# Performance work log

Measured on AMD Instinct MI355X. Metric: run time of the kernel, lower is better.

The kernel has to match this reference:

```python
import jax, jax.numpy as jnp
import numpy as np
import math

SEQLEN, DIM, N_HEADS = 2048, 4096, 32
HEAD_DIM = DIM // N_HEADS
NEG_INF = -1e30  # exp underflows to exactly 0, same effect as -inf without NaN risk


def setup_inputs() -> dict:
    key = jax.random.key(0)
    ks = jax.random.split(key, 7)
    scale = 1.0 / math.sqrt(DIM)
    x = jax.random.normal(ks[0], (SEQLEN, DIM), dtype=jnp.float32)
    weight_q = jax.random.normal(ks[1], (DIM, DIM), dtype=jnp.float32) * scale
    weight_k = jax.random.normal(ks[2], (DIM, DIM), dtype=jnp.float32) * scale
    weight_v = jax.random.normal(ks[3], (DIM, DIM), dtype=jnp.float32) * scale
    weight_o = jax.random.normal(ks[4], (DIM, DIM), dtype=jnp.float32) * scale
    # RoPE frequencies: freqs_cis = exp(i * t * theta_j), standard LLaMA schedule
    inv_freq = 1.0 / (10000.0 ** (np.arange(0, HEAD_DIM, 2, dtype=np.float32) / HEAD_DIM))
    angles = np.arange(SEQLEN, dtype=np.float32)[:, None] * inv_freq[None, :]  # [S, hd/2]
    freqs_cos = jnp.asarray(np.cos(angles), dtype=jnp.float32)
    freqs_sin = jnp.asarray(np.sin(angles), dtype=jnp.float32)
    # additive causal mask [S, S]
    mask = jnp.where(jnp.triu(jnp.ones((SEQLEN, SEQLEN), dtype=bool), k=1), NEG_INF, 0.0).astype(jnp.float32)
    return {"x": x, "weight_q": weight_q, "weight_k": weight_k, "weight_v": weight_v,
            "weight_o": weight_o, "freqs_cos": freqs_cos, "freqs_sin": freqs_sin,
            "mask": mask, "start_pos": 0}


def _apply_rope(t, cos, sin):
    # t: [S, H, hd]; cos/sin: [S, hd/2]
    tr = t.reshape(*t.shape[:-1], -1, 2)           # [S, H, hd/2, 2]
    t_re, t_im = tr[..., 0], tr[..., 1]
    c = cos[:, None, :]
    s = sin[:, None, :]
    out_re = t_re * c - t_im * s
    out_im = t_re * s + t_im * c
    return jnp.stack([out_re, out_im], axis=-1).reshape(t.shape)


def reference(x, weight_q, weight_k, weight_v, weight_o, freqs_cos, freqs_sin, mask, start_pos):
    S, D = x.shape
    hd = freqs_cos.shape[-1] * 2
    H = D // hd
    # the per-head double loop over wq[j][i] is exactly a full [D,D] projection
    xq = (x @ weight_q).reshape(S, H, hd)
    xk = (x @ weight_k).reshape(S, H, hd)
    xv = (x @ weight_v).reshape(S, H, hd)
    xq = _apply_rope(xq, freqs_cos, freqs_sin)
    xk = _apply_rope(xk, freqs_cos, freqs_sin)
    # start_pos == 0 prefill: cache slice == freshly computed keys/values
    scores = jnp.einsum('shd,thd->hst', xq, xk) / jnp.sqrt(jnp.float32(hd))
    scores = scores + mask[None, :, :]
    probs = jax.nn.softmax(scores.astype(jnp.float32), axis=-1).astype(xq.dtype)
    qkv = jnp.einsum('hst,thd->shd', probs, xv).reshape(S, D)
    return qkv @ weight_o
```

## Files before the change

### kernel.cpp

```cpp
#include <hip/hip_runtime.h>
#include <hip/hip_bf16.h>
#include <type_traits>

typedef __hip_bfloat16 bf16;
typedef __attribute__((ext_vector_type(8))) short s8v;
typedef __attribute__((ext_vector_type(4))) short s4v;
typedef __attribute__((ext_vector_type(4))) float f4v;

#define MFMA16(A, B, C) __builtin_amdgcn_mfma_f32_16x16x32_bf16((A), (B), (C), 0, 0, 0)

constexpr int SEQ = 2048;
constexpr int DIM = 4096;
constexpr int NH  = 32;
constexpr int HD  = 128;

__device__ __forceinline__ short f2bs(float f) {
    __hip_bfloat16_raw r = __float2bfloat16(f);
    return (short)r.x;
}

__device__ __forceinline__ void ld_g2l(const bf16* g, bf16* l) {
    __builtin_amdgcn_global_load_lds(
        (const __attribute__((address_space(1))) void*)g,
        (__attribute__((address_space(3))) void*)l, 16, 0, 0);
}

__global__ void convert_bf16(const float* __restrict__ s, bf16* __restrict__ d) {
    int i = blockIdx.x * blockDim.x + threadIdx.x;
    float4 f = ((const float4*)s)[i];
    s4v o;
    o[0] = f2bs(f.x); o[1] = f2bs(f.y); o[2] = f2bs(f.z); o[3] = f2bs(f.w);
    *(s4v*)(d + (size_t)i * 4) = o;
}

__global__ __launch_bounds__(256) void convt_bf16(const float* __restrict__ src,
                                                  bf16* __restrict__ dst,
                                                  int R, int C) {
    __shared__ float t[64][65];
    const int c0 = blockIdx.x * 64, r0 = blockIdx.y * 64;
    const int tid = threadIdx.x;
    const int lr = tid >> 4;
    const int lc = (tid & 15) * 4;
#pragma unroll
    for (int i = 0; i < 4; i++) {
        float4 f = *(const float4*)(src + (size_t)(r0 + lr + 16 * i) * C + c0 + lc);
        t[lr + 16 * i][lc]     = f.x;
        t[lr + 16 * i][lc + 1] = f.y;
        t[lr + 16 * i][lc + 2] = f.z;
        t[lr + 16 * i][lc + 3] = f.w;
    }
    __syncthreads();
    const int oc = tid >> 2;
#pragma unroll
    for (int i = 0; i < 2; i++) {
        int rr = (tid & 3) * 8 + 32 * i;
        s8v o;
#pragma unroll
        for (int e = 0; e < 8; e++) o[e] = f2bs(t[rr + e][oc]);
        *(s8v*)(dst + (size_t)(c0 + oc) * R + r0 + rr) = o;
    }
}

template <typename CT>
__global__ __launch_bounds__(512, 2) void gemm_256(const bf16* __restrict__ A,
                                                   const bf16* __restrict__ Bt,
                                                   CT* __restrict__ C,
                                                   int K, size_t cstride) {
    __shared__ bf16 As_[2][256 * 64];
    __shared__ bf16 Bs_[2][256 * 64];
    const int tid  = threadIdx.x;
    const int lane = tid & 63;
    const int wv   = tid >> 6;
    const int m16  = lane & 15;
    const int quad = lane >> 4;
    const int wm   = wv >> 2, wn = wv & 3;

    const int NBN = (int)gridDim.x;
    const int lin = (int)(blockIdx.y * gridDim.x + blockIdx.x);
    const int nw8 = (int)(gridDim.x * gridDim.y) >> 3;
    const int nv  = (lin & 7) * nw8 + (lin >> 3);
    const int bm  = nv / NBN;
    const int bn  = nv - bm * NBN;

    const bf16* Ab = A  + (size_t)bm * 256 * K;
    const bf16* Bb = Bt + (size_t)bn * 256 * K;

    const int row0 = tid >> 3;
    const int gc8  = ((tid & 7) ^ (row0 & 7)) * 8;
    const int dst0 = wv * 512;
    const int dst1 = 4096 + wv * 512;

    const int aB  = (wm * 128 + m16) * 64;
    const int bB  = (wn * 64 + m16) * 64;
    const int swz = m16 & 7;
    const int c0k = ((0 + quad) ^ swz) * 8;
    const int c1k = ((4 + quad) ^ swz) * 8;

    const int NT = K >> 6;

    f4v acc[8][4] = {};
    s8v aR[4][2], bR[4][2];

#define STAGEH(gb, lb) do { \
        ld_g2l((gb) + (size_t)row0 * K + gc8, (lb) + dst0); \
        ld_g2l((gb) + (size_t)(row0 + 64) * K + gc8, (lb) + dst1); } while (0)
#define LDA_(i, ks)  aR[i][ks] = *(const s8v*)(Ac + aB + (i) * 1024 + ((ks) ? c1k : c0k))
#define LDAU_(i, ks) aR[i][ks] = *(const s8v*)(Ac + aB + (i) * 1024 + 4096 + ((ks) ? c1k : c0k))
#define LDB_(j, ks)  bR[j][ks] = *(const s8v*)(Bc + bB + (j) * 1024 + ((ks) ? c1k : c0k))
#define MMQ(ai, i, j) do { acc[ai][j] = MFMA16(aR[i][0], bR[j][0], acc[ai][j]); \
                           acc[ai][j] = MFMA16(aR[i][1], bR[j][1], acc[ai][j]); } while (0)
#define BARX()  __builtin_amdgcn_s_barrier()
#define LGKM0() do { asm volatile("s_waitcnt lgkmcnt(0)" ::: "memory"); \
                     __builtin_amdgcn_sched_barrier(0); } while (0)

    STAGEH(Ab, As_[0]); STAGEH(Ab + (size_t)128 * K, As_[0] + 8192);
    STAGEH(Bb, Bs_[0]); STAGEH(Bb + (size_t)128 * K, Bs_[0] + 8192);
    STAGEH(Ab + 64, As_[1]); STAGEH(Ab + (size_t)128 * K + 64, As_[1] + 8192);
    STAGEH(Bb + 64, Bs_[1]); STAGEH(Bb + (size_t)128 * K + 64, Bs_[1] + 8192);
    asm volatile("s_waitcnt vmcnt(8)" ::: "memory");
    __builtin_amdgcn_sched_barrier(0);
    BARX();

    for (int t = 0; t < NT; ++t) {
        const int cur = t & 1;
        const bf16* Ac = As_[cur];
        const bf16* Bc = Bs_[cur];
        const bool more = (t + 2 < NT);
        const int k2 = (t + 2) << 6;

        LDA_(0, 0); LDA_(0, 1); LDA_(1, 0); LDA_(1, 1);
        LDA_(2, 0); LDA_(2, 1); LDA_(3, 0); LDA_(3, 1);
        LDB_(0, 0); LDB_(0, 1); LDB_(1, 0); LDB_(1, 1);
        BARX(); LGKM0();
        __builtin_amdgcn_s_setprio(1);
        MMQ(0, 0, 0); MMQ(0, 0, 1); MMQ(1, 1, 0); MMQ(1, 1, 1);
        MMQ(2, 2, 0); MMQ(2, 2, 1); MMQ(3, 3, 0); MMQ(3, 3, 1);
        __builtin_amdgcn_s_setprio(0);
        BARX();

        LDB_(2, 0); LDB_(2, 1); LDB_(3, 0); LDB_(3, 1);
        BARX(); LGKM0();
        __builtin_amdgcn_s_setprio(1);
        MMQ(0, 0, 2); MMQ(0, 0, 3); MMQ(1, 1, 2); MMQ(1, 1, 3);
        MMQ(2, 2, 2); MMQ(2, 2, 3); MMQ(3, 3, 2); MMQ(3, 3, 3);
        __builtin_amdgcn_s_setprio(0);
        BARX();

        LDAU_(0, 0); LDAU_(0, 1); LDAU_(1, 0); LDAU_(1, 1);
        LDAU_(2, 0); LDAU_(2, 1); LDAU_(3, 0); LDAU_(3, 1);
        if (more) {
            STAGEH(Bb + k2, Bs_[cur]);
            STAGEH(Bb + (size_t)128 * K + k2, Bs_[cur] + 8192);
        }
        BARX(); LGKM0();
        __builtin_amdgcn_s_setprio(1);
        MMQ(4, 0, 0); MMQ(4, 0, 1); MMQ(5, 1, 0); MMQ(5, 1, 1);
        MMQ(6, 2, 0); MMQ(6, 2, 1); MMQ(7, 3, 0); MMQ(7, 3, 1);
        __builtin_amdgcn_s_setprio(0);
        BARX();

        if (more) {
            STAGEH(Ab + k2, As_[cur]);
            STAGEH(Ab + (size_t)128 * K + k2, As_[cur] + 8192);
            asm volatile("s_waitcnt vmcnt(8)" ::: "memory");
        } else {
            asm volatile("s_waitcnt vmcnt(0)" ::: "memory");
        }
        __builtin_amdgcn_sched_barrier(0);
        BARX();
        __builtin_amdgcn_s_setprio(1);
        MMQ(4, 0, 2); MMQ(4, 0, 3); MMQ(5, 1, 2); MMQ(5, 1, 3);
        MMQ(6, 2, 2); MMQ(6, 2, 3); MMQ(7, 3, 2); MMQ(7, 3, 3);
        __builtin_amdgcn_s_setprio(0);
        BARX();
    }

#undef STAGEH
#undef LDA_
#undef LDAU_
#undef LDB_
#undef MMQ
#undef BARX
#undef LGKM0

#pragma unroll
    for (int i = 0; i < 8; i++)
#pragma unroll
        for (int j = 0; j < 4; j++)
#pragma unroll
            for (int r = 0; r < 4; r++) {
                int row = bm * 256 + wm * 128 + i * 16 + quad * 4 + r;
                int ct  = bn * 256 + wn * 64 + j * 16 + m16;
                CT* dst = C + (size_t)(ct >> 12) * cstride + (size_t)row * DIM + (ct & 4095);
                if constexpr (std::is_same<CT, float>::value)
                    *dst = acc[i][j][r];
                else
                    *dst = __float2bfloat16(acc[i][j][r]);
            }
}

template <typename AT, typename CT>
__global__ __launch_bounds__(256) void gemm_nat(const AT* __restrict__ A,
                                                const float* __restrict__ B,
                                                CT* __restrict__ C,
                                                int M, int N, int K) {
    __shared__ short As[128][40];
    __shared__ short Bs[128][40];
    const int tid  = threadIdx.x;
    const int lane = tid & 63;
    const int w    = tid >> 6;
    const int m16  = lane & 15;
    const int quad = lane >> 4;
    const int wm   = w >> 1, wn = w & 1;
    const int bm   = blockIdx.y, bn = blockIdx.x;

    const AT* Ab = A + (size_t)bm * 128 * K;

    f4v acc[4][4] = {};
    const int r0 = tid >> 2;
    const int kc = (tid & 3) * 8;

    for (int k0 = 0; k0 < K; k0 += 32) {
        if constexpr (std::is_same<AT, float>::value) {
#pragma unroll
            for (int half = 0; half < 2; half++) {
                const float* src = Ab + (size_t)(r0 + 64 * half) * K + k0 + kc;
                float4 f0 = *(const float4*)(src);
                float4 f1 = *(const float4*)(src + 4);
                s8v t;
                t[0] = f2bs(f0.x); t[1] = f2bs(f0.y); t[2] = f2bs(f0.z); t[3] = f2bs(f0.w);
                t[4] = f2bs(f1.x); t[5] = f2bs(f1.y); t[6] = f2bs(f1.z); t[7] = f2bs(f1.w);
                *(s8v*)&As[r0 + 64 * half][kc] = t;
            }
        } else {
            *(s8v*)&As[r0][kc]      = *(const s8v*)(Ab + (size_t)r0 * K + k0 + kc);
            *(s8v*)&As[r0 + 64][kc] = *(const s8v*)(Ab + (size_t)(r0 + 64) * K + k0 + kc);
        }
#pragma unroll
        for (int v = tid; v < 512; v += 256) {
            int kr = v >> 4;
            int nc = (v & 15) * 8;
            const float* src = B + (size_t)(k0 + kr) * N + bn * 128 + nc;
            float4 f0 = *(const float4*)(src);
            float4 f1 = *(const float4*)(src + 4);
            Bs[nc + 0][kr] = f2bs(f0.x); Bs[nc + 1][kr] = f2bs(f0.y);
            Bs[nc + 2][kr] = f2bs(f0.z); Bs[nc + 3][kr] = f2bs(f0.w);
            Bs[nc + 4][kr] = f2bs(f1.x); Bs[nc + 5][kr] = f2bs(f1.y);
            Bs[nc + 6][kr] = f2bs(f1.z); Bs[nc + 7][kr] = f2bs(f1.w);
        }
        __syncthreads();

        s8v a[4], b[4];
#pragma unroll
        for (int i = 0; i < 4; i++) a[i] = *(s8v*)&As[wm * 64 + i * 16 + m16][quad * 8];
#pragma unroll
        for (int j = 0; j < 4; j++) b[j] = *(s8v*)&Bs[wn * 64 + j * 16 + m16][quad * 8];
#pragma unroll
        for (int i = 0; i < 4; i++)
#pragma unroll
            for (int j = 0; j < 4; j++) acc[i][j] = MFMA16(a[i], b[j], acc[i][j]);
        __syncthreads();
    }

#pragma unroll
    for (int i = 0; i < 4; i++)
#pragma unroll
        for (int j = 0; j < 4; j++)
#pragma unroll
            for (int r = 0; r < 4; r++) {
                int row = bm * 128 + wm * 64 + i * 16 + quad * 4 + r;
                int col = bn * 128 + wn * 64 + j * 16 + m16;
                if constexpr (std::is_same<CT, float>::value)
                    C[(size_t)row * N + col] = acc[i][j][r];
                else
                    C[(size_t)row * N + col] = __float2bfloat16(acc[i][j][r]);
            }
}

__global__ void rope_kernel(bf16* __restrict__ Q, bf16* __restrict__ K,
                            const float* __restrict__ fc, const float* __restrict__ fs) {
    int tid = blockIdx.x * blockDim.x + threadIdx.x;
    int s = tid >> 11;
    int r = tid & 2047;
    int i = r & 63;
    float c  = fc[s * 64 + i];
    float sn = fs[s * 64 + i];
    size_t idx = (size_t)s * DIM + 2 * r;
    float qre = __bfloat162float(Q[idx]), qim = __bfloat162float(Q[idx + 1]);
    Q[idx]     = __float2bfloat16(qre * c - qim * sn);
    Q[idx + 1] = __float2bfloat16(qre * sn + qim * c);
    float kre = __bfloat162float(K[idx]), kim = __bfloat162float(K[idx + 1]);
    K[idx]     = __float2bfloat16(kre * c - kim * sn);
    K[idx + 1] = __float2bfloat16(kre * sn + kim * c);
}

__global__ __launch_bounds__(256) void attn_kernel(const bf16* __restrict__ Q,
                                                   const bf16* __restrict__ K,
                                                   const bf16* __restrict__ V,
                                                   bf16* __restrict__ O) {
    __shared__ short Ks[64][136];
    __shared__ short Vs[128][72];
    __shared__ short Ps[64][72];

    const int p  = blockIdx.x;
    const int h  = blockIdx.y;
    const int tid  = threadIdx.x;
    const int w    = tid >> 6;
    const int lane = tid & 63;
    const int m16  = lane & 15;
    const int quad = lane >> 4;
    const float scale = 0.08838834764831845f;
    const int NQB = (int)gridDim.x * 2;

    const int rn  = tid >> 4;
    const int rc  = (tid & 15) * 8;
    const int dcs = (tid & 15) & 7;

    for (int half = 0; half < 2; half++) {
        const int qb = half ? (NQB - 1 - p) : p;

        s8v aq[4];
        {
            const bf16* qp = Q + (size_t)(qb * 64 + w * 16 + m16) * DIM + h * HD + quad * 8;
#pragma unroll
            for (int ks = 0; ks < 4; ks++) aq[ks] = *(const s8v*)(qp + ks * 32);
        }

        f4v acc[8] = {};
        float mrow[4] = {-1e30f, -1e30f, -1e30f, -1e30f};
        float lrow[4] = {};

        s8v kreg[4], vreg[4];
        {
            const bf16* kp = K + (size_t)rn * DIM + h * HD + rc;
            const bf16* vp = V + (size_t)rn * DIM + h * HD + rc;
#pragma unroll
            for (int it = 0; it < 4; it++) {
                kreg[it] = *(const s8v*)(kp + (size_t)it * 16 * DIM);
                vreg[it] = *(const s8v*)(vp + (size_t)it * 16 * DIM);
            }
        }

        for (int kt = 0; kt <= qb; kt++) {
#pragma unroll
            for (int it = 0; it < 4; it++)
                *(s8v*)&Ks[it * 16 + rn][rc] = kreg[it];
#pragma unroll
            for (int it = 0; it < 4; it++) {
                int n   = it * 16 + rn;
                int col = (((n >> 3) ^ dcs) << 3) | (n & 7);
#pragma unroll
                for (int e = 0; e < 8; e++) Vs[rc + e][col] = vreg[it][e];
            }
            __syncthreads();

            if (kt < qb) {
                const bf16* kp = K + (size_t)((kt + 1) * 64 + rn) * DIM + h * HD + rc;
                const bf16* vp = V + (size_t)((kt + 1) * 64 + rn) * DIM + h * HD + rc;
#pragma unroll
                for (int it = 0; it < 4; it++) {
                    kreg[it] = *(const s8v*)(kp + (size_t)it * 16 * DIM);
                    vreg[it] = *(const s8v*)(vp + (size_t)it * 16 * DIM);
                }
            }

            f4v sc[4] = {};
#pragma unroll
            for (int j = 0; j < 4; j++)
#pragma unroll
                for (int ks = 0; ks < 4; ks++) {
                    s8v bk = *(s8v*)&Ks[j * 16 + m16][ks * 32 + quad * 8];
                    sc[j] = MFMA16(aq[ks], bk, sc[j]);
                }

            const bool diag = (kt == qb);
#pragma unroll
            for (int j = 0; j < 4; j++)
#pragma unroll
                for (int r = 0; r < 4; r++) {
                    float sv = sc[j][r] * scale;
                    if (diag && (j * 16 + m16) > (w * 16 + quad * 4 + r)) sv = -1e30f;
                    sc[j][r] = sv;
                }

#pragma unroll
            for (int r = 0; r < 4; r++) {
                float mx = fmaxf(fmaxf(sc[0][r], sc[1][r]), fmaxf(sc[2][r], sc[3][r]));
#pragma unroll
                for (int off = 1; off < 16; off <<= 1) mx = fmaxf(mx, __shfl_xor(mx, off, 64));
                float mn    = fmaxf(mrow[r], mx);
                float alpha = __expf(mrow[r] - mn);
                mrow[r] = mn;
                float rs = 0.f;
#pragma unroll
                for (int j = 0; j < 4; j++) {
                    float pj = __expf(sc[j][r] - mn);
                    sc[j][r] = pj;
                    rs += pj;
                }
#pragma unroll
                for (int off = 1; off < 16; off <<= 1) rs += __shfl_xor(rs, off, 64);
                lrow[r] = lrow[r] * alpha + rs;
#pragma unroll
                for (int jo = 0; jo < 8; jo++) acc[jo][r] = acc[jo][r] * alpha;
            }

#pragma unroll
            for (int j = 0; j < 4; j++)
#pragma unroll
                for (int r = 0; r < 4; r++)
                    Ps[w * 16 + quad * 4 + r][j * 16 + m16] = f2bs(sc[j][r]);
            asm volatile("s_waitcnt lgkmcnt(0)" ::: "memory");
            __builtin_amdgcn_sched_barrier(0);

#pragma unroll
            for (int ks2 = 0; ks2 < 2; ks2++) {
                s8v ap = *(s8v*)&Ps[w * 16 + m16][ks2 * 32 + quad * 8];
#pragma unroll
                for (int jo = 0; jo < 8; jo++) {
                    int dv = jo * 16 + m16;
                    int cg = (((ks2 * 4 + quad) ^ ((dv >> 3) & 7)) << 3);
                    s8v bv = *(s8v*)&Vs[dv][cg];
                    acc[jo] = MFMA16(ap, bv, acc[jo]);
                }
            }
            __syncthreads();
        }

#pragma unroll
        for (int jo = 0; jo < 8; jo++)
#pragma unroll
            for (int r = 0; r < 4; r++) {
                float o = acc[jo][r] / fmaxf(lrow[r], 1e-30f);
                int row = qb * 64 + w * 16 + quad * 4 + r;
                int col = h * HD + jo * 16 + m16;
                O[(size_t)row * DIM + col] = __float2bfloat16(o);
            }
    }
}

extern "C" void kernel_launch(void* const* d_in, const int* in_sizes, int n_in,
                              void* d_out, int out_size, void* d_ws, size_t ws_size,
                              hipStream_t stream) {
    const float* x  = (const float*)d_in[0];
    const float* wq = (const float*)d_in[1];
    const float* wk = (const float*)d_in[2];
    const float* wv = (const float*)d_in[3];
    const float* wo = (const float*)d_in[4];
    const float* fc = (const float*)d_in[5];
    const float* fs = (const float*)d_in[6];

    float* out = (float*)d_out;

    const size_t SZ = (size_t)SEQ * DIM;
    const size_t WZ = (size_t)DIM * DIM;
    bf16* Q  = (bf16*)d_ws;
    bf16* Kb = Q + SZ;
    bf16* V  = Kb + SZ;
    bf16* AO = V + SZ;

    const size_t needF = (5 * SZ + 3 * WZ) * sizeof(bf16);
    const size_t needU = (5 * SZ + WZ) * sizeof(bf16);

    dim3 tGw(DIM / 64, DIM / 64);

    if (ws_size >= needF) {
        bf16* xb = AO + SZ;
        bf16* wb = xb + SZ;

        convert_bf16<<<(int)(SZ / 4 / 256), 256, 0, stream>>>(x, xb);
        convt_bf16<<<tGw, 256, 0, stream>>>(wq, wb, DIM, DIM);
        convt_bf16<<<tGw, 256, 0, stream>>>(wk, wb + WZ, DIM, DIM);
        convt_bf16<<<tGw, 256, 0, stream>>>(wv, wb + 2 * WZ, DIM, DIM);

        gemm_256<bf16><<<dim3(3 * DIM / 256, SEQ / 256), 512, 0, stream>>>(
            xb, wb, Q, DIM, SZ);

        rope_kernel<<<(SEQ * (DIM / 2)) / 256, 256, 0, stream>>>(Q, Kb, fc, fs);
        attn_kernel<<<dim3(SEQ / 128, NH), 256, 0, stream>>>(Q, Kb, V, AO);

        convt_bf16<<<tGw, 256, 0, stream>>>(wo, wb, DIM, DIM);
        gemm_256<float><<<dim3(DIM / 256, SEQ / 256), 512, 0, stream>>>(
            AO, wb, out, DIM, 0);
    } else if (ws_size >= needU) {
        bf16* xb = AO + SZ;
        bf16* wb = xb + SZ;

        dim3 gU(DIM / 256, SEQ / 256);

        convert_bf16<<<(int)(SZ / 4 / 256), 256, 0, stream>>>(x, xb);

        convt_bf16<<<tGw, 256, 0, stream>>>(wq, wb, DIM, DIM);
        gemm_256<bf16><<<gU, 512, 0, stream>>>(xb, wb, Q, DIM, 0);
        convt_bf16<<<tGw, 256, 0, stream>>>(wk, wb, DIM, DIM);
        gemm_256<bf16><<<gU, 512, 0, stream>>>(xb, wb, Kb, DIM, 0);
        convt_bf16<<<tGw, 256, 0, stream>>>(wv, wb, DIM, DIM);
        gemm_256<bf16><<<gU, 512, 0, stream>>>(xb, wb, V, DIM, 0);

        rope_kernel<<<(SEQ * (DIM / 2)) / 256, 256, 0, stream>>>(Q, Kb, fc, fs);
        attn_kernel<<<dim3(SEQ / 128, NH), 256, 0, stream>>>(Q, Kb, V, AO);

        convt_bf16<<<tGw, 256, 0, stream>>>(wo, wb, DIM, DIM);
        gemm_256<float><<<gU, 512, 0, stream>>>(AO, wb, out, DIM, 0);
    } else {
        dim3 gGn(DIM / 128, SEQ / 128);
        gemm_nat<float, bf16><<<gGn, 256, 0, stream>>>(x, wq, Q,  SEQ, DIM, DIM);
        gemm_nat<float, bf16><<<gGn, 256, 0, stream>>>(x, wk, Kb, SEQ, DIM, DIM);
        gemm_nat<float, bf16><<<gGn, 256, 0, stream>>>(x, wv, V,  SEQ, DIM, DIM);
        rope_kernel<<<(SEQ * (DIM / 2)) / 256, 256, 0, stream>>>(Q, Kb, fc, fs);
        attn_kernel<<<dim3(SEQ / 128, NH), 256, 0, stream>>>(Q, Kb, V, AO);
        gemm_nat<bf16, float><<<gGn, 256, 0, stream>>>(AO, wo, out, SEQ, DIM, DIM);
    }
}
```

Baseline: 822.0 us.

## Restructure GEMM into register-pipelined inner loop and narrower output-projection tiles

Measured after the change: 779.5 us. 1.05x faster.

```diff
diff --git a/kernel.cpp b/kernel.cpp
--- a/kernel.cpp
+++ b/kernel.cpp
@@ -61,13 +61,14 @@
     }
 }
 
-template <typename CT>
-__global__ __launch_bounds__(512, 2) void gemm_256(const bf16* __restrict__ A,
-                                                   const bf16* __restrict__ Bt,
-                                                   CT* __restrict__ C,
-                                                   int K, size_t cstride) {
+template <int NJ, typename CT>
+__global__ __launch_bounds__(512, 2) void gemm_pipe(const bf16* __restrict__ A,
+                                                    const bf16* __restrict__ Bt,
+                                                    CT* __restrict__ C,
+                                                    int K, size_t cstride) {
+    constexpr int BN = NJ * 64;
     __shared__ bf16 As_[2][256 * 64];
-    __shared__ bf16 Bs_[2][256 * 64];
+    __shared__ bf16 Bs_[2][BN * 64];
     const int tid  = threadIdx.x;
     const int lane = tid & 63;
     const int wv   = tid >> 6;
@@ -76,14 +77,14 @@
     const int wm   = wv >> 2, wn = wv & 3;
 
     const int NBN = (int)gridDim.x;
+    const int cpx = NBN >> 3;
     const int lin = (int)(blockIdx.y * gridDim.x + blockIdx.x);
-    const int nw8 = (int)(gridDim.x * gridDim.y) >> 3;
-    const int nv  = (lin & 7) * nw8 + (lin >> 3);
-    const int bm  = nv / NBN;
-    const int bn  = nv - bm * NBN;
+    const int s_  = lin >> 3;
+    const int bm  = s_ / cpx;
+    const int bn  = (lin & 7) * cpx + (s_ - bm * cpx);
 
     const bf16* Ab = A  + (size_t)bm * 256 * K;
-    const bf16* Bb = Bt + (size_t)bn * 256 * K;
+    const bf16* Bb = Bt + (size_t)bn * BN * K;
 
     const int row0 = tid >> 3;
     const int gc8  = ((tid & 7) ^ (row0 & 7)) * 8;
@@ -91,106 +92,105 @@
     const int dst1 = 4096 + wv * 512;
 
     const int aB  = (wm * 128 + m16) * 64;
-    const int bB  = (wn * 64 + m16) * 64;
+    const int bB  = (wn * (NJ * 16) + m16) * 64;
     const int swz = m16 & 7;
     const int c0k = ((0 + quad) ^ swz) * 8;
     const int c1k = ((4 + quad) ^ swz) * 8;
 
     const int NT = K >> 6;
 
-    f4v acc[8][4] = {};
-    s8v aR[4][2], bR[4][2];
+    f4v acc[8][NJ] = {};
+    s8v aF[2][2];
+    s8v bF[NJ][2];
 
 #define STAGEH(gb, lb) do { \
         ld_g2l((gb) + (size_t)row0 * K + gc8, (lb) + dst0); \
         ld_g2l((gb) + (size_t)(row0 + 64) * K + gc8, (lb) + dst1); } while (0)
-#define LDA_(i, ks)  aR[i][ks] = *(const s8v*)(Ac + aB + (i) * 1024 + ((ks) ? c1k : c0k))
-#define LDAU_(i, ks) aR[i][ks] = *(const s8v*)(Ac + aB + (i) * 1024 + 4096 + ((ks) ? c1k : c0k))
-#define LDB_(j, ks)  bR[j][ks] = *(const s8v*)(Bc + bB + (j) * 1024 + ((ks) ? c1k : c0k))
-#define MMQ(ai, i, j) do { acc[ai][j] = MFMA16(aR[i][0], bR[j][0], acc[ai][j]); \
-                           acc[ai][j] = MFMA16(aR[i][1], bR[j][1], acc[ai][j]); } while (0)
-#define BARX()  __builtin_amdgcn_s_barrier()
-#define LGKM0() do { asm volatile("s_waitcnt lgkmcnt(0)" ::: "memory"); \
-                     __builtin_amdgcn_sched_barrier(0); } while (0)
-
-    STAGEH(Ab, As_[0]); STAGEH(Ab + (size_t)128 * K, As_[0] + 8192);
-    STAGEH(Bb, Bs_[0]); STAGEH(Bb + (size_t)128 * K, Bs_[0] + 8192);
-    STAGEH(Ab + 64, As_[1]); STAGEH(Ab + (size_t)128 * K + 64, As_[1] + 8192);
-    STAGEH(Bb + 64, Bs_[1]); STAGEH(Bb + (size_t)128 * K + 64, Bs_[1] + 8192);
-    asm volatile("s_waitcnt vmcnt(8)" ::: "memory");
-    __builtin_amdgcn_sched_barrier(0);
-    BARX();
+#define STA(k0, buf) do { \
+        STAGEH(Ab + (k0), As_[buf]); \
+        STAGEH(Ab + (size_t)128 * K + (k0), As_[buf] + 8192); } while (0)
+#define STB(k0, buf) do { \
+        STAGEH(Bb + (k0), Bs_[buf]); \
+        if constexpr (NJ == 4) { \
+            STAGEH(Bb + (size_t)128 * K + (k0), Bs_[buf] + 8192); } } while (0)
+#define WAIT_VM_N() do { \
+        if constexpr (NJ == 4) asm volatile("s_waitcnt vmcnt(8)" ::: "memory"); \
+        else                   asm volatile("s_waitcnt vmcnt(6)" ::: "memory"); \
+        __builtin_amdgcn_sched_barrier(0); } while (0)
+#define ISSUE_NEXT(nb) do { \
+        _Pragma("unroll") \
+        for (int j = 0; j < NJ; ++j) { \
+            bF[j][0] = *(const s8v*)(Bs_[nb] + bB + j * 1024 + c0k); \
+            bF[j][1] = *(const s8v*)(Bs_[nb] + bB + j * 1024 + c1k); } \
+        aF[0][0] = *(const s8v*)(As_[nb] + aB + c0k); \
+        aF[0][1] = *(const s8v*)(As_[nb] + aB + c1k); } while (0)
+
+    STA(0, 0); STB(0, 0);
+    STA(64, 1); STB(64, 1);
+    WAIT_VM_N();
+    __builtin_amdgcn_s_barrier();
+    ISSUE_NEXT(0);
 
     for (int t = 0; t < NT; ++t) {
         const int cur = t & 1;
         const bf16* Ac = As_[cur];
-        const bf16* Bc = Bs_[cur];
+
+#pragma unroll
+        for (int i = 0; i < 7; ++i) {
+            aF[(i + 1) & 1][0] = *(const s8v*)(Ac + aB + (i + 1) * 1024 + c0k);
+            aF[(i + 1) & 1][1] = *(const s8v*)(Ac + aB + (i + 1) * 1024 + c1k);
+            asm volatile("s_waitcnt lgkmcnt(2)" ::: "memory");
+            __builtin_amdgcn_sched_barrier(0);
+            __builtin_amdgcn_s_setprio(1);
+#pragma unroll
+            for (int j = 0; j < NJ; ++j) {
+                acc[i][j] = MFMA16(aF[i & 1][0], bF[j][0], acc[i][j]);
+                acc[i][j] = MFMA16(aF[i & 1][1], bF[j][1], acc[i][j]);
+            }
+            __builtin_amdgcn_s_setprio(0);
+        }
+
+        asm volatile("s_waitcnt lgkmcnt(0)" ::: "memory");
+        __builtin_amdgcn_sched_barrier(0);
+        __builtin_amdgcn_s_barrier();
         const bool more = (t + 2 < NT);
-        const int k2 = (t + 2) << 6;
-
-        LDA_(0, 0); LDA_(0, 1); LDA_(1, 0); LDA_(1, 1);
-        LDA_(2, 0); LDA_(2, 1); LDA_(3, 0); LDA_(3, 1);
-        LDB_(0, 0); LDB_(0, 1); LDB_(1, 0); LDB_(1, 1);
-        BARX(); LGKM0();
+        if (more) {
+            const int k2 = (t + 2) << 6;
+            STA(k2, cur); STB(k2, cur);
+        }
         __builtin_amdgcn_s_setprio(1);
-        MMQ(0, 0, 0); MMQ(0, 0, 1); MMQ(1, 1, 0); MMQ(1, 1, 1);
-        MMQ(2, 2, 0); MMQ(2, 2, 1); MMQ(3, 3, 0); MMQ(3, 3, 1);
+#pragma unroll
+        for (int j = 0; j < NJ; ++j) {
+            acc[7][j] = MFMA16(aF[1][0], bF[j][0], acc[7][j]);
+            acc[7][j] = MFMA16(aF[1][1], bF[j][1], acc[7][j]);
+        }
         __builtin_amdgcn_s_setprio(0);
-        BARX();
-
-        LDB_(2, 0); LDB_(2, 1); LDB_(3, 0); LDB_(3, 1);
-        BARX(); LGKM0();
-        __builtin_amdgcn_s_setprio(1);
-        MMQ(0, 0, 2); MMQ(0, 0, 3); MMQ(1, 1, 2); MMQ(1, 1, 3);
-        MMQ(2, 2, 2); MMQ(2, 2, 3); MMQ(3, 3, 2); MMQ(3, 3, 3);
-        __builtin_amdgcn_s_setprio(0);
-        BARX();
-
-        LDAU_(0, 0); LDAU_(0, 1); LDAU_(1, 0); LDAU_(1, 1);
-        LDAU_(2, 0); LDAU_(2, 1); LDAU_(3, 0); LDAU_(3, 1);
         if (more) {
-            STAGEH(Bb + k2, Bs_[cur]);
-            STAGEH(Bb + (size_t)128 * K + k2, Bs_[cur] + 8192);
-        }
-        BARX(); LGKM0();
-        __builtin_amdgcn_s_setprio(1);
-        MMQ(4, 0, 0); MMQ(4, 0, 1); MMQ(5, 1, 0); MMQ(5, 1, 1);
-        MMQ(6, 2, 0); MMQ(6, 2, 1); MMQ(7, 3, 0); MMQ(7, 3, 1);
-        __builtin_amdgcn_s_setprio(0);
-        BARX();
-
-        if (more) {
-            STAGEH(Ab + k2, As_[cur]);
-            STAGEH(Ab + (size_t)128 * K + k2, As_[cur] + 8192);
-            asm volatile("s_waitcnt vmcnt(8)" ::: "memory");
-        } else {
+            WAIT_VM_N();
+        } else if (t + 1 < NT) {
             asm volatile("s_waitcnt vmcnt(0)" ::: "memory");
-        }
-        __builtin_amdgcn_sched_barrier(0);
-        BARX();
-        __builtin_amdgcn_s_setprio(1);
-        MMQ(4, 0, 2); MMQ(4, 0, 3); MMQ(5, 1, 2); MMQ(5, 1, 3);
-        MMQ(6, 2, 2); MMQ(6, 2, 3); MMQ(7, 3, 2); MMQ(7, 3, 3);
-        __builtin_amdgcn_s_setprio(0);
-        BARX();
+            __builtin_amdgcn_sched_barrier(0);
+        }
+        if (t + 1 < NT) {
+            __builtin_amdgcn_s_barrier();
+            ISSUE_NEXT(cur ^ 1);
+        }
     }
 
 #undef STAGEH
-#undef LDA_
-#undef LDAU_
-#undef LDB_
-#undef MMQ
-#undef BARX
-#undef LGKM0
+#undef STA
+#undef STB
+#undef WAIT_VM_N
+#undef ISSUE_NEXT
 
 #pragma unroll
     for (int i = 0; i < 8; i++)
 #pragma unroll
-        for (int j = 0; j < 4; j++)
+        for (int j = 0; j < NJ; j++)
 #pragma unroll
             for (int r = 0; r < 4; r++) {
                 int row = bm * 256 + wm * 128 + i * 16 + quad * 4 + r;
-                int ct  = bn * 256 + wn * 64 + j * 16 + m16;
+                int ct  = bn * BN + wn * (NJ * 16) + j * 16 + m16;
                 CT* dst = C + (size_t)(ct >> 12) * cstride + (size_t)row * DIM + (ct & 4095);
                 if constexpr (std::is_same<CT, float>::value)
                     *dst = acc[i][j][r];
@@ -473,14 +473,14 @@
         convt_bf16<<<tGw, 256, 0, stream>>>(wk, wb + WZ, DIM, DIM);
         convt_bf16<<<tGw, 256, 0, stream>>>(wv, wb + 2 * WZ, DIM, DIM);
 
-        gemm_256<bf16><<<dim3(3 * DIM / 256, SEQ / 256), 512, 0, stream>>>(
+        gemm_pipe<4, bf16><<<dim3(3 * DIM / 256, SEQ / 256), 512, 0, stream>>>(
             xb, wb, Q, DIM, SZ);
 
         rope_kernel<<<(SEQ * (DIM / 2)) / 256, 256, 0, stream>>>(Q, Kb, fc, fs);
         attn_kernel<<<dim3(SEQ / 128, NH), 256, 0, stream>>>(Q, Kb, V, AO);
 
         convt_bf16<<<tGw, 256, 0, stream>>>(wo, wb, DIM, DIM);
-        gemm_256<float><<<dim3(DIM / 256, SEQ / 256), 512, 0, stream>>>(
+        gemm_pipe<2, float><<<dim3(DIM / 128, SEQ / 256), 512, 0, stream>>>(
             AO, wb, out, DIM, 0);
     } else if (ws_size >= needU) {
         bf16* xb = AO + SZ;
@@ -491,17 +491,18 @@
         convert_bf16<<<(int)(SZ / 4 / 256), 256, 0, stream>>>(x, xb);
 
         convt_bf16<<<tGw, 256, 0, stream>>>(wq, wb, DIM, DIM);
-        gemm_256<bf16><<<gU, 512, 0, stream>>>(xb, wb, Q, DIM, 0);
+        gemm_pipe<4, bf16><<<gU, 512, 0, stream>>>(xb, wb, Q, DIM, 0);
         convt_bf16<<<tGw, 256, 0, stream>>>(wk, wb, DIM, DIM);
-        gemm_256<bf16><<<gU, 512, 0, stream>>>(xb, wb, Kb, DIM, 0);
+        gemm_pipe<4, bf16><<<gU, 512, 0, stream>>>(xb, wb, Kb, DIM, 0);
         convt_bf16<<<tGw, 256, 0, stream>>>(wv, wb, DIM, DIM);
-        gemm_256<bf16><<<gU, 512, 0, stream>>>(xb, wb, V, DIM, 0);
+        gemm_pipe<4, bf16><<<gU, 512, 0, stream>>>(xb, wb, V, DIM, 0);
 
         rope_kernel<<<(SEQ * (DIM / 2)) / 256, 256, 0, stream>>>(Q, Kb, fc, fs);
         attn_kernel<<<dim3(SEQ / 128, NH), 256, 0, stream>>>(Q, Kb, V, AO);
 
         convt_bf16<<<tGw, 256, 0, stream>>>(wo, wb, DIM, DIM);
-        gemm_256<float><<<gU, 512, 0, stream>>>(AO, wb, out, DIM, 0);
+        gemm_pipe<2, float><<<dim3(DIM / 128, SEQ / 256), 512, 0, stream>>>(
+            AO, wb, out, DIM, 0);
     } else {
         dim3 gGn(DIM / 128, SEQ / 128);
         gemm_nat<float, bf16><<<gGn, 256, 0, stream>>>(x, wq, Q,  SEQ, DIM, DIM);
```
